# Optimization experiments

Measured on AMD Instinct MI355X. Metric: run time of the kernel, lower is better.

## Reference

```python
import jax, jax.numpy as jnp
import numpy as np

N_NODES = 50000
N_EDGES = 800000
IN_DIM = 64
OUT_DIM = 64
N_GRAPHS = 64
EPS = 1e-16  # PyG softmax eps


def setup_inputs() -> dict:
    key = jax.random.key(0)
    ks = jax.random.split(key, 12)
    x = jax.random.normal(ks[0], (N_NODES, IN_DIM), dtype=jnp.float32)
    edge_index = jax.random.randint(ks[1], (2, N_EDGES), 0, N_NODES, dtype=jnp.int64)
    batch = jnp.sort(jax.random.randint(ks[2], (N_NODES,), 0, N_GRAPHS, dtype=jnp.int64))
    s = 1.0 / np.sqrt(IN_DIM)
    Wq = jax.random.normal(ks[3], (IN_DIM, OUT_DIM), dtype=jnp.float32) * s
    bq = jnp.zeros((OUT_DIM,), dtype=jnp.float32)
    Wk = jax.random.normal(ks[4], (IN_DIM, OUT_DIM), dtype=jnp.float32) * s
    bk = jnp.zeros((OUT_DIM,), dtype=jnp.float32)
    Wv = jax.random.normal(ks[5], (IN_DIM, OUT_DIM), dtype=jnp.float32) * s
    bv = jnp.zeros((OUT_DIM,), dtype=jnp.float32)
    Wskip = jax.random.normal(ks[6], (IN_DIM, OUT_DIM), dtype=jnp.float32) * s
    bskip = jnp.zeros((OUT_DIM,), dtype=jnp.float32)
    return {"x": x, "edge_index": edge_index, "batch": batch,
            "Wq": Wq, "bq": bq, "Wk": Wk, "bk": bk, "Wv": Wv, "bv": bv,
            "Wskip": Wskip, "bskip": bskip}


def _global_encoder(x, edge_index, batch, Wq, bq, Wk, bk, Wv, bv, Wskip, bskip):
    src, dst = edge_index[0], edge_index[1]  # messages flow src -> dst
    q = x @ Wq + bq                          # [N, D]
    k = x @ Wk + bk
    v = x @ Wv + bv
    qi = q[dst]                              # [E, D] gather at target
    kj = k[src]                              # [E, D] gather at source
    vj = v[src]
    logits = jnp.sum(qi * kj, axis=-1) / jnp.sqrt(jnp.float32(OUT_DIM))  # [E]
    # segment softmax over incoming edges of each dst node
    m = jax.ops.segment_max(logits, dst, num_segments=N_NODES)           # [N]
    m = jnp.where(jnp.isfinite(m), m, 0.0)
    e = jnp.exp(logits - m[dst])                                         # [E]
    denom = jax.ops.segment_sum(e, dst, num_segments=N_NODES)            # [N]
    alpha = e / (denom[dst] + EPS)                                       # [E]
    agg = jax.ops.segment_sum(alpha[:, None] * vj, dst, num_segments=N_NODES)  # [N, D]
    out = agg + (x @ Wskip + bskip)          # root/skip connection
    out = jax.nn.relu(out)
    # global mean pool over graphs
    sums = jax.ops.segment_sum(out, batch, num_segments=N_GRAPHS)        # [B, D]
    cnt = jax.ops.segment_sum(jnp.ones((x.shape[0],), out.dtype), batch, num_segments=N_GRAPHS)
    return sums / jnp.maximum(cnt, 1.0)[:, None]


def reference(x, edge_index, batch, Wq, bq, Wk, bk, Wv, bv, Wskip, bskip):
    return _global_encoder(x, edge_index, batch, Wq, bq, Wk, bk, Wv, bv, Wskip, bskip)
```

## Files before the change

kernel.cpp:

```cpp
#include <hip/hip_runtime.h>

#define D64 64
#define EPS 1e-16f

__global__ __launch_bounds__(256) void qkvs_kernel(
    const float* __restrict__ x,
    const float* __restrict__ Wq, const float* __restrict__ bq,
    const float* __restrict__ Wk, const float* __restrict__ bk,
    const float* __restrict__ Wv, const float* __restrict__ bv,
    const float* __restrict__ Ws, const float* __restrict__ bs,
    float* __restrict__ q, float* __restrict__ k, float* __restrict__ v,
    float* __restrict__ skip, int n_nodes)
{
    __shared__ float wq[4096], wk[4096], wv[4096];
    __shared__ float xs[16 * 64];
    __shared__ float bqs[64], bks[64], bvs[64], bss[64];
    int t = threadIdx.x;
    for (int i = t; i < 1024; i += 256) {
        ((float4*)wq)[i] = ((const float4*)Wq)[i];
        ((float4*)wk)[i] = ((const float4*)Wk)[i];
        ((float4*)wv)[i] = ((const float4*)Wv)[i];
    }
    if (t < 64) { bqs[t] = bq[t]; bks[t] = bk[t]; bvs[t] = bv[t]; bss[t] = bs[t]; }
    __syncthreads();

    int d  = t & 63;
    int j0 = t >> 6;
    int ntiles = (n_nodes + 15) / 16;
    for (int tile = blockIdx.x; tile < ntiles; tile += gridDim.x) {
        int base = tile * 16;
        __syncthreads();
        if (base + 16 <= n_nodes) {
            ((float4*)xs)[t] = ((const float4*)x)[(size_t)base * 16 + t];
        } else {
            for (int i = t; i < 1024; i += 256) {
                int node = base + (i >> 6);
                xs[i] = (node < n_nodes) ? x[(size_t)node * 64 + (i & 63)] : 0.0f;
            }
        }
        __syncthreads();

        float aq[4], ak[4], av[4], asv[4];
        #pragma unroll
        for (int j = 0; j < 4; ++j) { aq[j] = bqs[d]; ak[j] = bks[d]; av[j] = bvs[d]; asv[j] = bss[d]; }
        #pragma unroll 8
        for (int i = 0; i < 64; ++i) {
            float w0 = wq[i * 64 + d];
            float w1 = wk[i * 64 + d];
            float w2 = wv[i * 64 + d];
            float w3 = Ws[i * 64 + d];
            #pragma unroll
            for (int j = 0; j < 4; ++j) {
                float xi = xs[(j0 * 4 + j) * 64 + i];
                aq[j]  += xi * w0;
                ak[j]  += xi * w1;
                av[j]  += xi * w2;
                asv[j] += xi * w3;
            }
        }
        #pragma unroll
        for (int j = 0; j < 4; ++j) {
            int node = base + j0 * 4 + j;
            if (node < n_nodes) {
                size_t o = (size_t)node * 64 + d;
                q[o] = aq[j]; k[o] = ak[j]; v[o] = av[j]; skip[o] = asv[j];
            }
        }
    }
}

__global__ __launch_bounds__(256) void hist_kernel(
    const int* __restrict__ dst, int* __restrict__ deg, int E)
{
    int e = blockIdx.x * 256 + threadIdx.x;
    if (e < E) atomicAdd(deg + dst[e], 1);
}

__global__ __launch_bounds__(1024) void scan_kernel(
    const int* __restrict__ deg, int* __restrict__ rowstart, int N, int E)
{
    __shared__ int sums[1024];
    int t = threadIdx.x;
    int chunk = (N + 1023) >> 10;
    int beg = t * chunk;
    int end = min(beg + chunk, N);
    int s = 0;
    for (int i = beg; i < end; ++i) s += deg[i];
    sums[t] = s;
    __syncthreads();
    for (int off = 1; off < 1024; off <<= 1) {
        int add = (t >= off) ? sums[t - off] : 0;
        __syncthreads();
        sums[t] += add;
        __syncthreads();
    }
    int prefix = (t == 0) ? 0 : sums[t - 1];
    for (int i = beg; i < end; ++i) { rowstart[i] = prefix; prefix += deg[i]; }
    if (t == 0) rowstart[N] = E;
}

__global__ __launch_bounds__(256) void fill_kernel(
    const int* __restrict__ src, const int* __restrict__ dst,
    const int* __restrict__ rowstart, int* __restrict__ cursor,
    int* __restrict__ srcs, int E)
{
    int e = blockIdx.x * 256 + threadIdx.x;
    if (e >= E) return;
    int d = dst[e];
    int pos = rowstart[d] + atomicAdd(cursor + d, 1);
    srcs[pos] = src[e];
}

__global__ __launch_bounds__(256) void attn_gather_kernel(
    const float* __restrict__ q, const float* __restrict__ k,
    const float* __restrict__ v, const float* __restrict__ skip,
    const int* __restrict__ rowstart, const int* __restrict__ srcs,
    const int* __restrict__ batch,
    float* __restrict__ out, float* __restrict__ cnt, int N)
{
    int t = threadIdx.x;
    int l = t & 15;
    int node = (blockIdx.x * 256 + t) >> 4;
    bool valid = node < N;

    float4 qv = make_float4(0.f, 0.f, 0.f, 0.f);
    int p0 = 0, p1 = 0;
    if (valid) {
        qv = ((const float4*)q)[(size_t)node * 16 + l];
        p0 = rowstart[node];
        p1 = rowstart[node + 1];
    }

    float4 acc = make_float4(0.f, 0.f, 0.f, 0.f);
    float den = 0.f;
    float m = -INFINITY;

    for (int p = p0; p < p1; ++p) {
        int s = srcs[p];
        float4 kj = ((const float4*)k)[(size_t)s * 16 + l];
        float dp = qv.x * kj.x + qv.y * kj.y + qv.z * kj.z + qv.w * kj.w;
        dp += __shfl_xor(dp, 1);
        dp += __shfl_xor(dp, 2);
        dp += __shfl_xor(dp, 4);
        dp += __shfl_xor(dp, 8);
        float logit = dp * 0.125f;
        float4 vj = ((const float4*)v)[(size_t)s * 16 + l];
        if (logit > m) {
            float sc = __expf(m - logit);
            den *= sc; acc.x *= sc; acc.y *= sc; acc.z *= sc; acc.w *= sc;
            m = logit;
        }
        float ev = __expf(logit - m);
        den += ev;
        acc.x += ev * vj.x; acc.y += ev * vj.y;
        acc.z += ev * vj.z; acc.w += ev * vj.w;
    }

    float4 val = make_float4(0.f, 0.f, 0.f, 0.f);
    int g = -1;
    if (valid) {
        float inv = 1.0f / (den + EPS);
        float4 sk = ((const float4*)skip)[(size_t)node * 16 + l];
        val.x = fmaxf(acc.x * inv + sk.x, 0.f);
        val.y = fmaxf(acc.y * inv + sk.y, 0.f);
        val.z = fmaxf(acc.z * inv + sk.z, 0.f);
        val.w = fmaxf(acc.w * inv + sk.w, 0.f);
        g = batch[node];
    }

    int g0 = __shfl(g, 0);
    bool uni = __all(g == g0);
    if (uni) {
        if (g0 >= 0) {
            val.x += __shfl_xor(val.x, 16); val.x += __shfl_xor(val.x, 32);
            val.y += __shfl_xor(val.y, 16); val.y += __shfl_xor(val.y, 32);
            val.z += __shfl_xor(val.z, 16); val.z += __shfl_xor(val.z, 32);
            val.w += __shfl_xor(val.w, 16); val.w += __shfl_xor(val.w, 32);
            if ((t & 63) < 16) {
                float* o = out + (size_t)g0 * 64 + l * 4;
                atomicAdd(o + 0, val.x);
                atomicAdd(o + 1, val.y);
                atomicAdd(o + 2, val.z);
                atomicAdd(o + 3, val.w);
            }
            if ((t & 63) == 0) atomicAdd(cnt + g0, 4.0f);
        }
    } else if (valid) {
        float* o = out + (size_t)g * 64 + l * 4;
        atomicAdd(o + 0, val.x);
        atomicAdd(o + 1, val.y);
        atomicAdd(o + 2, val.z);
        atomicAdd(o + 3, val.w);
        if (l == 0) atomicAdd(cnt + g, 1.0f);
    }
}

__global__ __launch_bounds__(256) void pool_div_kernel(
    float* __restrict__ out, const float* __restrict__ cnt, int n)
{
    int idx = blockIdx.x * 256 + threadIdx.x;
    if (idx >= n) return;
    int g = idx >> 6;
    out[idx] /= fmaxf(cnt[g], 1.0f);
}

extern "C" void kernel_launch(void* const* d_in, const int* in_sizes, int n_in,
                              void* d_out, int out_size, void* d_ws, size_t ws_size,
                              hipStream_t stream) {
    const float* x     = (const float*)d_in[0];
    const int*   eidx  = (const int*)d_in[1];
    const int*   batch = (const int*)d_in[2];
    const float* Wq = (const float*)d_in[3];
    const float* bq = (const float*)d_in[4];
    const float* Wk = (const float*)d_in[5];
    const float* bk = (const float*)d_in[6];
    const float* Wv = (const float*)d_in[7];
    const float* bv = (const float*)d_in[8];
    const float* Ws = (const float*)d_in[9];
    const float* bs = (const float*)d_in[10];

    int N = in_sizes[0] / D64;
    int E = in_sizes[1] / 2;
    const int* src = eidx;
    const int* dst = eidx + E;

    char* w = (char*)d_ws;
    size_t NB = (size_t)N * D64 * sizeof(float);
    float* q    = (float*)(w);
    float* k    = (float*)(w + NB);
    float* v    = (float*)(w + 2 * NB);
    float* skip = (float*)(w + 3 * NB);
    char*  p    = w + 4 * NB;
    int*   deg      = (int*)p;                 p += (size_t)N * 4;
    int*   cursor   = (int*)p;                 p += (size_t)N * 4;
    int*   rowstart = (int*)p;                 p += (size_t)(N + 1) * 4;
    int*   srcs     = (int*)p;                 p += (size_t)E * 4;
    float* cnt      = (float*)p;

    hipMemsetAsync(deg, 0, 2 * (size_t)N * 4, stream);
    hipMemsetAsync(cnt, 0, 64 * sizeof(float), stream);
    hipMemsetAsync(d_out, 0, (size_t)out_size * sizeof(float), stream);

    qkvs_kernel<<<512, 256, 0, stream>>>(x, Wq, bq, Wk, bk, Wv, bv, Ws, bs,
                                         q, k, v, skip, N);
    int blocks_e = (E + 255) / 256;
    hist_kernel<<<blocks_e, 256, 0, stream>>>(dst, deg, E);
    scan_kernel<<<1, 1024, 0, stream>>>(deg, rowstart, N, E);
    fill_kernel<<<blocks_e, 256, 0, stream>>>(src, dst, rowstart, cursor, srcs, E);
    int blocks_g = ((size_t)N * 16 + 255) / 256;
    attn_gather_kernel<<<blocks_g, 256, 0, stream>>>(q, k, v, skip, rowstart, srcs,
                                                     batch, (float*)d_out, cnt, N);
    pool_div_kernel<<<(out_size + 255) / 256, 256, 0, stream>>>((float*)d_out,
                                                                (const float*)cnt, out_size);
}
```

Baseline: 402.3 us.

## Fuse degree histogram into projection kernel and unroll attention gather by four

Folds the destination-degree histogram into the QKV/skip projection kernel as a grid-stride tail loop, which drops one launch. The projection grid goes from 512 to 1024 blocks. The attention gather loop is unrolled by four: it issues four independent K/V row loads at once and does a single online-softmax rescale per group of four edges, to get more memory-level parallelism. The cost is more register pressure, and the atomics are now serialized behind the GEMM work in each block.

Result: faster. 385.0 us (-4.3%).

```diff
diff --git a/kernel.cpp b/kernel.cpp
--- a/kernel.cpp
+++ b/kernel.cpp
@@ -2,6 +2,17 @@
 
 #define D64 64
 #define EPS 1e-16f
+
+__device__ __forceinline__ float dot4(float4 a, float4 b) {
+    return a.x * b.x + a.y * b.y + a.z * b.z + a.w * b.w;
+}
+__device__ __forceinline__ float rsum16(float p) {
+    p += __shfl_xor(p, 1);
+    p += __shfl_xor(p, 2);
+    p += __shfl_xor(p, 4);
+    p += __shfl_xor(p, 8);
+    return p;
+}
 
 __global__ __launch_bounds__(256) void qkvs_kernel(
     const float* __restrict__ x,
@@ -10,7 +21,8 @@
     const float* __restrict__ Wv, const float* __restrict__ bv,
     const float* __restrict__ Ws, const float* __restrict__ bs,
     float* __restrict__ q, float* __restrict__ k, float* __restrict__ v,
-    float* __restrict__ skip, int n_nodes)
+    float* __restrict__ skip, int n_nodes,
+    const int* __restrict__ dst, int* __restrict__ deg, int E)
 {
     __shared__ float wq[4096], wk[4096], wv[4096];
     __shared__ float xs[16 * 64];
@@ -67,13 +79,9 @@
             }
         }
     }
-}
-
-__global__ __launch_bounds__(256) void hist_kernel(
-    const int* __restrict__ dst, int* __restrict__ deg, int E)
-{
-    int e = blockIdx.x * 256 + threadIdx.x;
-    if (e < E) atomicAdd(deg + dst[e], 1);
+
+    for (int e = blockIdx.x * 256 + t; e < E; e += gridDim.x * 256)
+        atomicAdd(deg + dst[e], 1);
 }
 
 __global__ __launch_bounds__(1024) void scan_kernel(
@@ -135,19 +143,55 @@
     float den = 0.f;
     float m = -INFINITY;
 
-    for (int p = p0; p < p1; ++p) {
+    const float4* k4 = (const float4*)k;
+    const float4* v4 = (const float4*)v;
+
+    int p = p0;
+    for (; p + 4 <= p1; p += 4) {
+        int s0 = srcs[p + 0];
+        int s1 = srcs[p + 1];
+        int s2 = srcs[p + 2];
+        int s3 = srcs[p + 3];
+        float4 k0 = k4[(size_t)s0 * 16 + l];
+        float4 k1 = k4[(size_t)s1 * 16 + l];
+        float4 k2 = k4[(size_t)s2 * 16 + l];
+        float4 k3 = k4[(size_t)s3 * 16 + l];
+        float4 v0 = v4[(size_t)s0 * 16 + l];
+        float4 v1 = v4[(size_t)s1 * 16 + l];
+        float4 v2 = v4[(size_t)s2 * 16 + l];
+        float4 v3 = v4[(size_t)s3 * 16 + l];
+
+        float l0 = rsum16(dot4(qv, k0)) * 0.125f;
+        float l1 = rsum16(dot4(qv, k1)) * 0.125f;
+        float l2 = rsum16(dot4(qv, k2)) * 0.125f;
+        float l3 = rsum16(dot4(qv, k3)) * 0.125f;
+
+        float mx = fmaxf(fmaxf(l0, l1), fmaxf(l2, l3));
+        if (mx > m) {
+            float sc = __expf(m - mx);
+            den *= sc;
+            acc.x *= sc; acc.y *= sc; acc.z *= sc; acc.w *= sc;
+            m = mx;
+        }
+        float e0 = __expf(l0 - m);
+        float e1 = __expf(l1 - m);
+        float e2 = __expf(l2 - m);
+        float e3 = __expf(l3 - m);
+        den += (e0 + e1) + (e2 + e3);
+        acc.x += e0 * v0.x + e1 * v1.x + e2 * v2.x + e3 * v3.x;
+        acc.y += e0 * v0.y + e1 * v1.y + e2 * v2.y + e3 * v3.y;
+        acc.z += e0 * v0.z + e1 * v1.z + e2 * v2.z + e3 * v3.z;
+        acc.w += e0 * v0.w + e1 * v1.w + e2 * v2.w + e3 * v3.w;
+    }
+    for (; p < p1; ++p) {
         int s = srcs[p];
-        float4 kj = ((const float4*)k)[(size_t)s * 16 + l];
-        float dp = qv.x * kj.x + qv.y * kj.y + qv.z * kj.z + qv.w * kj.w;
-        dp += __shfl_xor(dp, 1);
-        dp += __shfl_xor(dp, 2);
-        dp += __shfl_xor(dp, 4);
-        dp += __shfl_xor(dp, 8);
-        float logit = dp * 0.125f;
-        float4 vj = ((const float4*)v)[(size_t)s * 16 + l];
+        float4 kj = k4[(size_t)s * 16 + l];
+        float4 vj = v4[(size_t)s * 16 + l];
+        float logit = rsum16(dot4(qv, kj)) * 0.125f;
         if (logit > m) {
             float sc = __expf(m - logit);
-            den *= sc; acc.x *= sc; acc.y *= sc; acc.z *= sc; acc.w *= sc;
+            den *= sc;
+            acc.x *= sc; acc.y *= sc; acc.z *= sc; acc.w *= sc;
             m = logit;
         }
         float ev = __expf(logit - m);
@@ -241,11 +285,10 @@
     hipMemsetAsync(cnt, 0, 64 * sizeof(float), stream);
     hipMemsetAsync(d_out, 0, (size_t)out_size * sizeof(float), stream);
 
-    qkvs_kernel<<<512, 256, 0, stream>>>(x, Wq, bq, Wk, bk, Wv, bv, Ws, bs,
-                                         q, k, v, skip, N);
+    qkvs_kernel<<<1024, 256, 0, stream>>>(x, Wq, bq, Wk, bk, Wv, bv, Ws, bs,
+                                          q, k, v, skip, N, dst, deg, E);
+    scan_kernel<<<1, 1024, 0, stream>>>(deg, rowstart, N, E);
     int blocks_e = (E + 255) / 256;
-    hist_kernel<<<blocks_e, 256, 0, stream>>>(dst, deg, E);
-    scan_kernel<<<1, 1024, 0, stream>>>(deg, rowstart, N, E);
     fill_kernel<<<blocks_e, 256, 0, stream>>>(src, dst, rowstart, cursor, srcs, E);
     int blocks_g = ((size_t)N * 16 + 255) / 256;
     attn_gather_kernel<<<blocks_g, 256, 0, stream>>>(q, k, v, skip, rowstart, srcs,
```

## Store K/V in bf16, split attention into logits and PV passes, fuse histogram

Applied to the files above, without the earlier changes.

K and V are written as bf16, which halves the bytes moved by the random per-edge gathers. The fused online-softmax attention kernel becomes two passes. The first computes logits, row max and denominator with 4-edge unrolling; the second reads the stored logits and accumulates V with 4-way unrolled independent loads. The degree histogram is folded into the QKV projection kernel, the grid is doubled, and the memsets are merged. This adds an E-sized logits buffer plus a second pass over srcs, and bf16 K/V introduces rounding error.

New measurement: 403.3 us. Within noise of the previous version (+0.3%).

```diff
diff --git a/kernel.cpp b/kernel.cpp
--- a/kernel.cpp
+++ b/kernel.cpp
@@ -2,6 +2,28 @@
 
 #define D64 64
 #define EPS 1e-16f
+
+typedef unsigned int uint;
+typedef uint uivec2 __attribute__((ext_vector_type(2)));
+
+__device__ __forceinline__ float bf_lo(uint u) { return __uint_as_float(u << 16); }
+__device__ __forceinline__ float bf_hi(uint u) { return __uint_as_float(u & 0xffff0000u); }
+__device__ __forceinline__ unsigned short f2bf(float f) {
+    uint u = __float_as_uint(f);
+    u += 0x7fffu + ((u >> 16) & 1u);
+    return (unsigned short)(u >> 16);
+}
+__device__ __forceinline__ float rsum16(float p) {
+    p += __shfl_xor(p, 1);
+    p += __shfl_xor(p, 2);
+    p += __shfl_xor(p, 4);
+    p += __shfl_xor(p, 8);
+    return p;
+}
+__device__ __forceinline__ float dotk(float4 q4, uivec2 w) {
+    return q4.x * bf_lo(w[0]) + q4.y * bf_hi(w[0]) +
+           q4.z * bf_lo(w[1]) + q4.w * bf_hi(w[1]);
+}
 
 __global__ __launch_bounds__(256) void qkvs_kernel(
     const float* __restrict__ x,
@@ -9,8 +31,10 @@
     const float* __restrict__ Wk, const float* __restrict__ bk,
     const float* __restrict__ Wv, const float* __restrict__ bv,
     const float* __restrict__ Ws, const float* __restrict__ bs,
-    float* __restrict__ q, float* __restrict__ k, float* __restrict__ v,
-    float* __restrict__ skip, int n_nodes)
+    float* __restrict__ q, unsigned short* __restrict__ kbuf,
+    unsigned short* __restrict__ vbuf,
+    float* __restrict__ skip, int n_nodes,
+    const int* __restrict__ dst, int* __restrict__ deg, int E)
 {
     __shared__ float wq[4096], wk[4096], wv[4096];
     __shared__ float xs[16 * 64];
@@ -63,17 +87,16 @@
             int node = base + j0 * 4 + j;
             if (node < n_nodes) {
                 size_t o = (size_t)node * 64 + d;
-                q[o] = aq[j]; k[o] = ak[j]; v[o] = av[j]; skip[o] = asv[j];
+                q[o]    = aq[j];
+                skip[o] = asv[j];
+                kbuf[o] = f2bf(ak[j]);
+                vbuf[o] = f2bf(av[j]);
             }
         }
     }
-}
-
-__global__ __launch_bounds__(256) void hist_kernel(
-    const int* __restrict__ dst, int* __restrict__ deg, int E)
-{
-    int e = blockIdx.x * 256 + threadIdx.x;
-    if (e < E) atomicAdd(deg + dst[e], 1);
+
+    for (int e = blockIdx.x * 256 + t; e < E; e += gridDim.x * 256)
+        atomicAdd(deg + dst[e], 1);
 }
 
 __global__ __launch_bounds__(1024) void scan_kernel(
@@ -111,49 +134,117 @@
     srcs[pos] = src[e];
 }
 
-__global__ __launch_bounds__(256) void attn_gather_kernel(
-    const float* __restrict__ q, const float* __restrict__ k,
-    const float* __restrict__ v, const float* __restrict__ skip,
+__global__ __launch_bounds__(256) void qk_logits_kernel(
+    const float* __restrict__ q, const uint* __restrict__ kbuf,
     const int* __restrict__ rowstart, const int* __restrict__ srcs,
-    const int* __restrict__ batch,
-    float* __restrict__ out, float* __restrict__ cnt, int N)
+    float* __restrict__ logits, float* __restrict__ mden, int N)
 {
     int t = threadIdx.x;
     int l = t & 15;
     int node = (blockIdx.x * 256 + t) >> 4;
     bool valid = node < N;
 
-    float4 qv = make_float4(0.f, 0.f, 0.f, 0.f);
+    float4 q4 = make_float4(0.f, 0.f, 0.f, 0.f);
     int p0 = 0, p1 = 0;
     if (valid) {
-        qv = ((const float4*)q)[(size_t)node * 16 + l];
+        q4 = ((const float4*)q)[(size_t)node * 16 + l];
         p0 = rowstart[node];
         p1 = rowstart[node + 1];
     }
 
+    float m = -INFINITY, den = 0.f;
+    const uivec2* k2 = (const uivec2*)kbuf;
+
+    int p = p0;
+    for (; p + 4 <= p1; p += 4) {
+        int s0 = srcs[p + 0]; int s1 = srcs[p + 1];
+        int s2 = srcs[p + 2]; int s3 = srcs[p + 3];
+        uivec2 w0 = k2[(size_t)s0 * 16 + l];
+        uivec2 w1 = k2[(size_t)s1 * 16 + l];
+        uivec2 w2 = k2[(size_t)s2 * 16 + l];
+        uivec2 w3 = k2[(size_t)s3 * 16 + l];
+        float l0 = rsum16(dotk(q4, w0)) * 0.125f;
+        float l1 = rsum16(dotk(q4, w1)) * 0.125f;
+        float l2 = rsum16(dotk(q4, w2)) * 0.125f;
+        float l3 = rsum16(dotk(q4, w3)) * 0.125f;
+        float mx = fmaxf(fmaxf(l0, l1), fmaxf(l2, l3));
+        if (mx > m) {
+            den *= __expf(m - mx);
+            m = mx;
+        }
+        den += __expf(l0 - m) + __expf(l1 - m) + __expf(l2 - m) + __expf(l3 - m);
+        if (l < 4) {
+            float lv = (l == 0) ? l0 : (l == 1) ? l1 : (l == 2) ? l2 : l3;
+            logits[p + l] = lv;
+        }
+    }
+    for (; p < p1; ++p) {
+        int s = srcs[p];
+        uivec2 w0 = k2[(size_t)s * 16 + l];
+        float lg = rsum16(dotk(q4, w0)) * 0.125f;
+        if (lg > m) {
+            den *= __expf(m - lg);
+            m = lg;
+        }
+        den += __expf(lg - m);
+        if (l == 0) logits[p] = lg;
+    }
+
+    if (valid && l == 0) {
+        mden[2 * (size_t)node + 0] = m;
+        mden[2 * (size_t)node + 1] = den;
+    }
+}
+
+__global__ __launch_bounds__(256) void pv_kernel(
+    const uint* __restrict__ vbuf, const float* __restrict__ skip,
+    const float* __restrict__ logits, const float* __restrict__ mden,
+    const int* __restrict__ rowstart, const int* __restrict__ srcs,
+    const int* __restrict__ batch,
+    float* __restrict__ out, float* __restrict__ cnt, int N)
+{
+    int t = threadIdx.x;
+    int l = t & 15;
+    int node = (blockIdx.x * 256 + t) >> 4;
+    bool valid = node < N;
+
+    int p0 = 0, p1 = 0;
+    float m = 0.f, den = 0.f;
+    if (valid) {
+        p0 = rowstart[node];
+        p1 = rowstart[node + 1];
+        m   = mden[2 * (size_t)node + 0];
+        den = mden[2 * (size_t)node + 1];
+    }
+
     float4 acc = make_float4(0.f, 0.f, 0.f, 0.f);
-    float den = 0.f;
-    float m = -INFINITY;
-
-    for (int p = p0; p < p1; ++p) {
+    const uivec2* v2 = (const uivec2*)vbuf;
+
+    int p = p0;
+    for (; p + 4 <= p1; p += 4) {
+        int s0 = srcs[p + 0]; int s1 = srcs[p + 1];
+        int s2 = srcs[p + 2]; int s3 = srcs[p + 3];
+        uivec2 w0 = v2[(size_t)s0 * 16 + l];
+        uivec2 w1 = v2[(size_t)s1 * 16 + l];
+        uivec2 w2 = v2[(size_t)s2 * 16 + l];
+        uivec2 w3 = v2[(size_t)s3 * 16 + l];
+        float e0 = __expf(logits[p + 0] - m);
+        float e1 = __expf(logits[p + 1] - m);
+        float e2 = __expf(logits[p + 2] - m);
+        float e3 = __expf(logits[p + 3] - m);
+        acc.x += e0 * bf_lo(w0[0]) + e1 * bf_lo(w1[0]) + e2 * bf_lo(w2[0]) + e3 * bf_lo(w3[0]);
+        acc.y += e0 * bf_hi(w0[0]) + e1 * bf_hi(w1[0]) + e2 * bf_hi(w2[0]) + e3 * bf_hi(w3[0]);
+        acc.z += e0 * bf_lo(w0[1]) + e1 * bf_lo(w1[1]) + e2 * bf_lo(w2[1]) + e3 * bf_lo(w3[1]);
+        acc.w += e0 * bf_hi(w0[1]) + e1 * bf_hi(w1[1]) + e2 * bf_hi(w2[1]) + e3 * bf_hi(w3[1]);
+    }
+    for (; p < p1; ++p) {
         int s = srcs[p];
-        float4 kj = ((const float4*)k)[(size_t)s * 16 + l];
-        float dp = qv.x * kj.x + qv.y * kj.y + qv.z * kj.z + qv.w * kj.w;
-        dp += __shfl_xor(dp, 1);
-        dp += __shfl_xor(dp, 2);
-        dp += __shfl_xor(dp, 4);
-        dp += __shfl_xor(dp, 8);
-        float logit = dp * 0.125f;
-        float4 vj = ((const float4*)v)[(size_t)s * 16 + l];
-        if (logit > m) {
-            float sc = __expf(m - logit);
-            den *= sc; acc.x *= sc; acc.y *= sc; acc.z *= sc; acc.w *= sc;
-            m = logit;
-        }
-        float ev = __expf(logit - m);
-        den += ev;
-        acc.x += ev * vj.x; acc.y += ev * vj.y;
-        acc.z += ev * vj.z; acc.w += ev * vj.w;
+        uivec2 w0 = v2[(size_t)s * 16 + l];
+        float ev = __expf(logits[p] - m);
+        acc.x += ev * bf_lo(w0[0]);
+        acc.y += ev * bf_hi(w0[0]);
+        acc.z += ev * bf_lo(w0[1]);
+        acc.w += ev * bf_hi(w0[1]);
     }
 
     float4 val = make_float4(0.f, 0.f, 0.f, 0.f);
@@ -226,30 +317,33 @@
 
     char* w = (char*)d_ws;
     size_t NB = (size_t)N * D64 * sizeof(float);
-    float* q    = (float*)(w);
-    float* k    = (float*)(w + NB);
-    float* v    = (float*)(w + 2 * NB);
-    float* skip = (float*)(w + 3 * NB);
-    char*  p    = w + 4 * NB;
+    float*          q    = (float*)(w);
+    float*          skip = (float*)(w + NB);
+    unsigned short* kbuf = (unsigned short*)(w + 2 * NB);
+    unsigned short* vbuf = (unsigned short*)(w + 2 * NB + NB / 2);
+    char* p = w + 3 * NB;
+    float* logits   = (float*)p;               p += (size_t)E * 4;
+    float* mden     = (float*)p;               p += 2 * (size_t)N * 4;
     int*   deg      = (int*)p;                 p += (size_t)N * 4;
     int*   cursor   = (int*)p;                 p += (size_t)N * 4;
+    float* cnt      = (float*)p;               p += 64 * 4;
     int*   rowstart = (int*)p;                 p += (size_t)(N + 1) * 4;
-    int*   srcs     = (int*)p;                 p += (size_t)E * 4;
-    float* cnt      = (float*)p;
-
-    hipMemsetAsync(deg, 0, 2 * (size_t)N * 4, stream);
-    hipMemsetAsync(cnt, 0, 64 * sizeof(float), stream);
-    hipMemsetAsync(d_out, 0, (size_t)out_size * sizeof(float), stream);
-
-    qkvs_kernel<<<512, 256, 0, stream>>>(x, Wq, bq, Wk, bk, Wv, bv, Ws, bs,
-                                         q, k, v, skip, N);
+    int*   srcs     = (int*)p;
+
+    (void)hipMemsetAsync(deg, 0, (2 * (size_t)N + 64) * 4, stream);
+    (void)hipMemsetAsync(d_out, 0, (size_t)out_size * sizeof(float), stream);
+
+    qkvs_kernel<<<1024, 256, 0, stream>>>(x, Wq, bq, Wk, bk, Wv, bv, Ws, bs,
+                                          q, kbuf, vbuf, skip, N, dst, deg, E);
+    scan_kernel<<<1, 1024, 0, stream>>>(deg, rowstart, N, E);
     int blocks_e = (E + 255) / 256;
-    hist_kernel<<<blocks_e, 256, 0, stream>>>(dst, deg, E);
-    scan_kernel<<<1, 1024, 0, stream>>>(deg, rowstart, N, E);
     fill_kernel<<<blocks_e, 256, 0, stream>>>(src, dst, rowstart, cursor, srcs, E);
     int blocks_g = ((size_t)N * 16 + 255) / 256;
-    attn_gather_kernel<<<blocks_g, 256, 0, stream>>>(q, k, v, skip, rowstart, srcs,
-                                                     batch, (float*)d_out, cnt, N);
+    qk_logits_kernel<<<blocks_g, 256, 0, stream>>>(q, (const uint*)kbuf, rowstart,
+                                                   srcs, logits, mden, N);
+    pv_kernel<<<blocks_g, 256, 0, stream>>>((const uint*)vbuf, skip, logits, mden,
+                                            rowstart, srcs, batch,
+                                            (float*)d_out, cnt, N);
     pool_div_kernel<<<(out_size + 255) / 256, 256, 0, stream>>>((float*)d_out,
                                                                 (const float*)cnt, out_size);
 }
```
